# Optimization experiments

Measured on AMD Instinct MI355X. Metric: run time of the kernel, lower is better.

## Reference

```python
import jax, jax.numpy as jnp
import numpy as np

B, S, D, H = 4, 2048, 1024, 16
HD = D // H

def setup_inputs() -> dict:
    key = jax.random.key(0)
    ks = jax.random.split(key, 11)
    s = 1.0 / np.sqrt(D)
    def lin(k):
        kw, kb = jax.random.split(k)
        return (jax.random.uniform(kw, (D, D), jnp.float32, -s, s),
                jax.random.uniform(kb, (D,), jnp.float32, -s, s))
    Wq, bq = lin(ks[0]); Wk, bk = lin(ks[1]); Wv, bv = lin(ks[2]); Wo, bo = lin(ks[3])
    return {
        "query": jax.random.normal(ks[4], (B, S, D), jnp.float32),
        "key": jax.random.normal(ks[5], (B, S, D), jnp.float32),
        "value": jax.random.normal(ks[6], (B, S, D), jnp.float32),
        "Wq": Wq, "bq": bq, "Wk": Wk, "bk": bk,
        "Wv": Wv, "bv": bv, "Wo": Wo, "bo": bo,
    }

def reference(query, key, value, Wq, bq, Wk, bk, Wv, bv, Wo, bo):
    def split_heads(x):  # [B,S,D] -> [B,H,S,HD]
        return x.reshape(B, S, H, HD).transpose(0, 2, 1, 3)
    q = split_heads(query @ Wq + bq)
    k = split_heads(key @ Wk + bk)
    v = split_heads(value @ Wv + bv)
    scores = jnp.einsum('bhqd,bhkd->bhqk', q, k) / np.sqrt(HD)
    probs = jax.nn.softmax(scores, axis=-1)
    ctx = jnp.einsum('bhqk,bhkd->bhqd', probs, v)
    ctx = ctx.transpose(0, 2, 1, 3).reshape(B, S, D)
    return ctx @ Wo + bo
```

## Files before the change

### kernel.cpp

```cpp
#include <hip/hip_runtime.h>
#include <hip/hip_bf16.h>

#define B_ 4
#define S_ 2048
#define D_ 1024
#define H_ 16
#define HD_ 64
#define M_ (B_*S_)

typedef __bf16 bf16;
typedef bf16 bf16x8 __attribute__((ext_vector_type(8)));
typedef bf16 bf16x4 __attribute__((ext_vector_type(4)));
typedef bf16 bf16x2 __attribute__((ext_vector_type(2)));
typedef float f32x4 __attribute__((ext_vector_type(4)));
typedef unsigned u32x4 __attribute__((ext_vector_type(4)));

__device__ __forceinline__ void gload_lds16(const void* g, void* l) {
  __builtin_amdgcn_global_load_lds((const __attribute__((address_space(1))) void*)g,
                                   (__attribute__((address_space(3))) void*)l, 16, 0, 0);
}

__device__ __forceinline__ unsigned pk2(float a, float b) {
  bf16x2 v;
  v[0] = (bf16)a; v[1] = (bf16)b;
  return __builtin_bit_cast(unsigned, v);
}

__global__ __launch_bounds__(256)
void wtrans_kernel(const float* __restrict__ Wq, const float* __restrict__ Wk,
                   const float* __restrict__ Wv, const float* __restrict__ Wo,
                   bf16* __restrict__ Wqt, bf16* __restrict__ Wkt,
                   bf16* __restrict__ Wvt, bf16* __restrict__ Wot) {
  __shared__ float tile[64][65];
  const float* W; bf16* Wt;
  switch (blockIdx.z) {
    case 0: W = Wq; Wt = Wqt; break;
    case 1: W = Wk; Wt = Wkt; break;
    case 2: W = Wv; Wt = Wvt; break;
    default: W = Wo; Wt = Wot; break;
  }
  int n0 = blockIdx.x * 64, k0 = blockIdx.y * 64;
  int tx = threadIdx.x & 63, ty = threadIdx.x >> 6;
#pragma unroll
  for (int i = 0; i < 16; i++) {
    int k = ty + i * 4;
    tile[k][tx] = W[(size_t)(k0 + k) * D_ + n0 + tx];
  }
  __syncthreads();
#pragma unroll
  for (int i = 0; i < 16; i++) {
    int n = ty + i * 4;
    Wt[(size_t)(n0 + n) * D_ + k0 + tx] = (bf16)tile[tx][n];
  }
}

__global__ __launch_bounds__(256)
void qkv_cvt_kernel(const float* __restrict__ q, const float* __restrict__ k,
                    const float* __restrict__ v,
                    bf16* __restrict__ qo, bf16* __restrict__ ko, bf16* __restrict__ vo) {
  const float* src; bf16* dst;
  switch (blockIdx.y) {
    case 0: src = q; dst = qo; break;
    case 1: src = k; dst = ko; break;
    default: src = v; dst = vo; break;
  }
  size_t i = ((size_t)blockIdx.x * 256 + threadIdx.x) * 8;
  f32x4 a = *(const f32x4*)(src + i);
  f32x4 b = *(const f32x4*)(src + i + 4);
  bf16x8 o;
  o[0] = (bf16)a[0]; o[1] = (bf16)a[1]; o[2] = (bf16)a[2]; o[3] = (bf16)a[3];
  o[4] = (bf16)b[0]; o[5] = (bf16)b[1]; o[6] = (bf16)b[2]; o[7] = (bf16)b[3];
  *(bf16x8*)(dst + i) = o;
}

#define QSCALE 0.18033688011112042f

__global__ __launch_bounds__(256)
void proj_gemm_kernel(const bf16* __restrict__ Aqb, const bf16* __restrict__ Akb,
                      const bf16* __restrict__ Avb,
                      const bf16* __restrict__ Wqt, const bf16* __restrict__ Wkt,
                      const bf16* __restrict__ Wvt,
                      const float* __restrict__ bq, const float* __restrict__ bk,
                      const float* __restrict__ bv,
                      bf16* __restrict__ qb, bf16* __restrict__ kb, bf16* __restrict__ vbT) {
  __shared__ bf16 As[128 * 64];
  __shared__ bf16 Bs[128 * 64];
  const bf16* A; const bf16* Bt; const float* bias;
  if (blockIdx.z == 0)      { A = Aqb; Bt = Wqt; bias = bq; }
  else if (blockIdx.z == 1) { A = Akb; Bt = Wkt; bias = bk; }
  else                      { A = Avb; Bt = Wvt; bias = bv; }

  const int orig = blockIdx.y * gridDim.x + blockIdx.x;
  const int swz  = (orig & 7) * 64 + (orig >> 3);
  const int n0 = (swz & 7) * 128, m0 = (swz >> 3) * 128;

  const int tid = threadIdx.x;
  const int lane = tid & 63, w = tid >> 6;
  const int wr = w >> 1, wc = w & 1;
  const int l15 = lane & 15, quad = lane >> 4;
  const int srow = lane >> 3, schunk = lane & 7;

  f32x4 acc[4][4] = {};

  for (int kt = 0; kt < D_ / 64; kt++) {
    const int k0 = kt * 64;
#pragma unroll
    for (int t = 0; t < 4; t++) {
      int r0 = w * 32 + t * 8;
      int row = r0 + srow;
      int cg = schunk ^ (row & 7);
      gload_lds16(A + (size_t)(m0 + row) * D_ + k0 + cg * 8, &As[r0 * 64]);
      gload_lds16(Bt + (size_t)(n0 + row) * D_ + k0 + cg * 8, &Bs[r0 * 64]);
    }
    __syncthreads();

#pragma unroll
    for (int ks = 0; ks < 2; ks++) {
      bf16x8 a[4], b[4];
#pragma unroll
      for (int fm = 0; fm < 4; fm++) {
        int row = wr * 64 + fm * 16 + l15;
        a[fm] = *(const bf16x8*)(&As[row * 64 + (((ks * 4 + quad) ^ (row & 7)) * 8)]);
      }
#pragma unroll
      for (int fn = 0; fn < 4; fn++) {
        int row = wc * 64 + fn * 16 + l15;
        b[fn] = *(const bf16x8*)(&Bs[row * 64 + (((ks * 4 + quad) ^ (row & 7)) * 8)]);
      }
#pragma unroll
      for (int fm = 0; fm < 4; fm++)
#pragma unroll
        for (int fn = 0; fn < 4; fn++)
          acc[fm][fn] = __builtin_amdgcn_mfma_f32_16x16x32_bf16(a[fm], b[fn], acc[fm][fn], 0, 0, 0);
    }
    __syncthreads();
  }

  if (blockIdx.z < 2) {
    bf16* C = (blockIdx.z == 0) ? qb : kb;
    float scale = (blockIdx.z == 0) ? QSCALE : 1.0f;
#pragma unroll
    for (int fm = 0; fm < 4; fm++) {
      int row = m0 + wr * 64 + fm * 16 + quad * 4;
#pragma unroll
      for (int fn = 0; fn < 4; fn++) {
        int col = n0 + wc * 64 + fn * 16 + l15;
        float bval = bias[col];
#pragma unroll
        for (int r = 0; r < 4; r++)
          C[(size_t)(row + r) * D_ + col] = (bf16)((acc[fm][fn][r] + bval) * scale);
      }
    }
  } else {
#pragma unroll
    for (int fm = 0; fm < 4; fm++) {
      int row = m0 + wr * 64 + fm * 16 + quad * 4;
#pragma unroll
      for (int fn = 0; fn < 4; fn++) {
        int col = n0 + wc * 64 + fn * 16 + l15;
        float bval = bias[col];
        bf16x4 pk;
#pragma unroll
        for (int r = 0; r < 4; r++) pk[r] = (bf16)(acc[fm][fn][r] + bval);
        *(bf16x4*)(vbT + (size_t)col * M_ + row) = pk;
      }
    }
  }
}

#define NT_ (S_ / 64)

__global__ __launch_bounds__(256)
void attn_kernel(const bf16* __restrict__ qb, const bf16* __restrict__ kb,
                 const bf16* __restrict__ vbT, bf16* __restrict__ ctxb) {
  __shared__ bf16 Ks[2][64 * 64];
  __shared__ bf16 Vs[3][64 * 64];

  const int orig = blockIdx.y * gridDim.x + blockIdx.x;
  const int swz  = (orig & 7) * 128 + (orig >> 3);
  const int bh = swz >> 4;
  const int b = bh >> 4, h = bh & 15;
  const int q0 = (swz & 15) * 128;

  const int tid = threadIdx.x, lane = tid & 63, w = tid >> 6;
  const int l15 = lane & 15, quad = lane >> 4;

  const size_t baseQ = ((size_t)(b * S_ + q0)) * D_ + h * HD_;

  bf16x8 qf[2][2];
#pragma unroll
  for (int fm = 0; fm < 2; fm++)
#pragma unroll
    for (int ks = 0; ks < 2; ks++)
      qf[fm][ks] = *(const bf16x8*)(qb + baseQ + (size_t)(w * 32 + fm * 16 + l15) * D_ + ks * 32 + quad * 8);

  bf16x8 vones;
#pragma unroll
  for (int i = 0; i < 8; i++) vones[i] = (bf16)1.0f;

  f32x4 o[2][4] = {};
  f32x4 o_l[2] = {};

  const int srow_i = lane >> 3;
  const int schunk = lane & 7;

  auto stage = [&](int kt) {
    if (kt >= NT_) return;
    const int kbuf = kt & 1, vbuf = kt % 3;
#pragma unroll
    for (int t = 0; t < 2; t++) {
      const int r0 = w * 16 + t * 8;
      const int row = r0 + srow_i;
      const int c = schunk ^ (row & 7);
      const bf16* gK = kb + ((size_t)(b * S_ + kt * 64 + row)) * D_ + h * 64 + c * 8;
      gload_lds16(gK, &Ks[kbuf][r0 * 64]);
      const bf16* gV = vbT + ((size_t)(h * 64 + row)) * M_ + b * S_ + kt * 64 + c * 8;
      gload_lds16(gV, &Vs[vbuf][r0 * 64]);
    }
  };

  auto QK = [&](f32x4 (&st)[4][2], int kbuf) {
#pragma unroll
    for (int fk = 0; fk < 4; fk++)
#pragma unroll
      for (int fq = 0; fq < 2; fq++) st[fk][fq] = f32x4{};
    __builtin_amdgcn_s_setprio(1);
#pragma unroll
    for (int ks = 0; ks < 2; ks++) {
#pragma unroll
      for (int fk = 0; fk < 4; fk++) {
        const int key = fk * 16 + l15;
        bf16x8 kf = *(const bf16x8*)(&Ks[kbuf][key * 64 + (((ks * 4 + quad) ^ (key & 7)) * 8)]);
#pragma unroll
        for (int fq = 0; fq < 2; fq++)
          st[fk][fq] = __builtin_amdgcn_mfma_f32_16x16x32_bf16(kf, qf[fq][ks], st[fk][fq], 0, 0, 0);
      }
    }
    __builtin_amdgcn_s_setprio(0);
  };

  auto FIN = [&](f32x4 (&st)[4][2], int vbuf) {
#pragma unroll
    for (int fk = 0; fk < 4; fk++)
#pragma unroll
      for (int fq = 0; fq < 2; fq++) {
        st[fk][fq][0] = __builtin_amdgcn_exp2f(st[fk][fq][0]);
        st[fk][fq][1] = __builtin_amdgcn_exp2f(st[fk][fq][1]);
        st[fk][fq][2] = __builtin_amdgcn_exp2f(st[fk][fq][2]);
        st[fk][fq][3] = __builtin_amdgcn_exp2f(st[fk][fq][3]);
      }
#pragma unroll
    for (int ks2 = 0; ks2 < 2; ks2++) {
      bf16x8 pf[2], vf[4];
#pragma unroll
      for (int fm = 0; fm < 2; fm++) {
        unsigned A0 = pk2(st[2 * ks2][fm][0], st[2 * ks2][fm][1]);
        unsigned A1 = pk2(st[2 * ks2][fm][2], st[2 * ks2][fm][3]);
        unsigned B0 = pk2(st[2 * ks2 + 1][fm][0], st[2 * ks2 + 1][fm][1]);
        unsigned B1 = pk2(st[2 * ks2 + 1][fm][2], st[2 * ks2 + 1][fm][3]);
        auto s0 = __builtin_amdgcn_permlane32_swap(A0, B0, false, false);
        auto s1 = __builtin_amdgcn_permlane32_swap(A1, B1, false, false);
        auto t0 = __builtin_amdgcn_permlane16_swap(s0[0], s0[1], false, false);
        auto t1 = __builtin_amdgcn_permlane16_swap(s1[0], s1[1], false, false);
        u32x4 wv;
        wv[0] = t0[0]; wv[1] = t1[0]; wv[2] = t0[1]; wv[3] = t1[1];
        pf[fm] = __builtin_bit_cast(bf16x8, wv);
      }
#pragma unroll
      for (int fd = 0; fd < 4; fd++) {
        const int d = fd * 16 + l15;
        vf[fd] = *(const bf16x8*)(&Vs[vbuf][d * 64 + (((ks2 * 4 + quad) ^ (d & 7)) * 8)]);
      }
      __builtin_amdgcn_s_setprio(1);
#pragma unroll
      for (int fm = 0; fm < 2; fm++) {
#pragma unroll
        for (int fd = 0; fd < 4; fd++)
          o[fm][fd] = __builtin_amdgcn_mfma_f32_16x16x32_bf16(pf[fm], vf[fd], o[fm][fd], 0, 0, 0);
        o_l[fm] = __builtin_amdgcn_mfma_f32_16x16x32_bf16(pf[fm], vones, o_l[fm], 0, 0, 0);
      }
      __builtin_amdgcn_s_setprio(0);
    }
  };

  f32x4 stA[4][2], stB[4][2];

  stage(0);
  __syncthreads();

  for (int i = 0; i < NT_ / 2; i++) {
    const int t = 2 * i;
    stage(t + 1);
    QK(stA, t & 1);
    if (i > 0) FIN(stB, (t - 1) % 3);
    __syncthreads();
    stage(t + 2);
    QK(stB, (t + 1) & 1);
    FIN(stA, t % 3);
    __syncthreads();
  }
  FIN(stB, (NT_ - 1) % 3);

#pragma unroll
  for (int fm = 0; fm < 2; fm++) {
#pragma unroll
    for (int r = 0; r < 4; r++) {
      float inv = 1.0f / o_l[fm][r];
      int row = w * 32 + fm * 16 + quad * 4 + r;
#pragma unroll
      for (int fd = 0; fd < 4; fd++)
        ctxb[baseQ + (size_t)row * D_ + fd * 16 + l15] = (bf16)(o[fm][fd][r] * inv);
    }
  }
}

__global__ __launch_bounds__(256)
void out_gemm_kernel(const bf16* __restrict__ A, const bf16* __restrict__ Bt,
                     const float* __restrict__ bias, float* __restrict__ Cout) {
  __shared__ bf16 As[128 * 64];
  __shared__ bf16 Bs[128 * 64];
  const int orig = blockIdx.y * gridDim.x + blockIdx.x;
  const int swz  = (orig & 7) * 64 + (orig >> 3);
  const int n0 = (swz & 7) * 128, m0 = (swz >> 3) * 128;

  const int tid = threadIdx.x;
  const int lane = tid & 63, w = tid >> 6;
  const int wr = w >> 1, wc = w & 1;
  const int l15 = lane & 15, quad = lane >> 4;
  const int srow = lane >> 3, schunk = lane & 7;

  f32x4 acc[4][4] = {};

  for (int kt = 0; kt < D_ / 64; kt++) {
    const int k0 = kt * 64;
#pragma unroll
    for (int t = 0; t < 4; t++) {
      int r0 = w * 32 + t * 8;
      int row = r0 + srow;
      int cg = schunk ^ (row & 7);
      gload_lds16(A + (size_t)(m0 + row) * D_ + k0 + cg * 8, &As[r0 * 64]);
      gload_lds16(Bt + (size_t)(n0 + row) * D_ + k0 + cg * 8, &Bs[r0 * 64]);
    }
    __syncthreads();

#pragma unroll
    for (int ks = 0; ks < 2; ks++) {
      bf16x8 a[4], b[4];
#pragma unroll
      for (int fm = 0; fm < 4; fm++) {
        int row = wr * 64 + fm * 16 + l15;
        a[fm] = *(const bf16x8*)(&As[row * 64 + (((ks * 4 + quad) ^ (row & 7)) * 8)]);
      }
#pragma unroll
      for (int fn = 0; fn < 4; fn++) {
        int row = wc * 64 + fn * 16 + l15;
        b[fn] = *(const bf16x8*)(&Bs[row * 64 + (((ks * 4 + quad) ^ (row & 7)) * 8)]);
      }
#pragma unroll
      for (int fm = 0; fm < 4; fm++)
#pragma unroll
        for (int fn = 0; fn < 4; fn++)
          acc[fm][fn] = __builtin_amdgcn_mfma_f32_16x16x32_bf16(a[fm], b[fn], acc[fm][fn], 0, 0, 0);
    }
    __syncthreads();
  }
#pragma unroll
  for (int fm = 0; fm < 4; fm++) {
    int row = m0 + wr * 64 + fm * 16 + quad * 4;
#pragma unroll
    for (int fn = 0; fn < 4; fn++) {
      int col = n0 + wc * 64 + fn * 16 + l15;
      float bval = bias[col];
#pragma unroll
      for (int r = 0; r < 4; r++)
        Cout[(size_t)(row + r) * D_ + col] = acc[fm][fn][r] + bval;
    }
  }
}

extern "C" void kernel_launch(void* const* d_in, const int* in_sizes, int n_in,
                              void* d_out, int out_size, void* d_ws, size_t ws_size,
                              hipStream_t stream) {
  const float* query = (const float*)d_in[0];
  const float* key   = (const float*)d_in[1];
  const float* value = (const float*)d_in[2];
  const float* Wq = (const float*)d_in[3];
  const float* bq = (const float*)d_in[4];
  const float* Wk = (const float*)d_in[5];
  const float* bk = (const float*)d_in[6];
  const float* Wv = (const float*)d_in[7];
  const float* bv = (const float*)d_in[8];
  const float* Wo = (const float*)d_in[9];
  const float* bo = (const float*)d_in[10];
  float* out = (float*)d_out;

  char* ws = (char*)d_ws;
  const size_t WT_BYTES = (size_t)D_ * D_ * sizeof(bf16);
  const size_t MD_BYTES = (size_t)M_ * D_ * sizeof(bf16);
  bf16* Wqt  = (bf16*)(ws);
  bf16* Wkt  = (bf16*)(ws + WT_BYTES);
  bf16* Wvt  = (bf16*)(ws + 2 * WT_BYTES);
  bf16* Wot  = (bf16*)(ws + 3 * WT_BYTES);
  bf16* qb   = (bf16*)(ws + 4 * WT_BYTES);
  bf16* kb   = (bf16*)(ws + 4 * WT_BYTES + MD_BYTES);
  bf16* vbT  = (bf16*)(ws + 4 * WT_BYTES + 2 * MD_BYTES);
  bf16* ctxb = (bf16*)(ws + 4 * WT_BYTES + 3 * MD_BYTES);
  bf16* qcv  = ctxb;
  bf16* kcv  = (bf16*)(ws + 4 * WT_BYTES + 4 * MD_BYTES);
  bf16* vcv  = (bf16*)(ws + 4 * WT_BYTES + 5 * MD_BYTES);

  wtrans_kernel<<<dim3(D_ / 64, D_ / 64, 4), 256, 0, stream>>>(
      Wq, Wk, Wv, Wo, Wqt, Wkt, Wvt, Wot);

  qkv_cvt_kernel<<<dim3((size_t)M_ * D_ / 2048, 3), 256, 0, stream>>>(
      query, key, value, qcv, kcv, vcv);

  proj_gemm_kernel<<<dim3(D_ / 128, M_ / 128, 3), 256, 0, stream>>>(
      qcv, kcv, vcv, Wqt, Wkt, Wvt, bq, bk, bv, qb, kb, vbT);

  attn_kernel<<<dim3(S_ / 128, B_ * H_), 256, 0, stream>>>(qb, kb, vbT, ctxb);

  out_gemm_kernel<<<dim3(D_ / 128, M_ / 128), 256, 0, stream>>>(ctxb, Wot, bo, out);
}
```

Measured before the change: 334.4 us.

## Fuse fp32-to-bf16 input conversion into projection GEMM A-tile loading

Removes the separate qkv conversion kernel. The projection GEMM now reads fp32 activations directly into registers, converts them to bf16 and writes them into swizzled LDS, with a register prefetch of the next k-tile that overlaps the MFMA compute. This avoids writing and re-reading three bf16 copies of the inputs and saves one kernel launch. In exchange, each GEMM tile reads twice the bytes of A from global memory because every N-tile reloads fp32, the kernel needs more registers, and there are two barriers per iteration.

```diff
diff --git a/kernel.cpp b/kernel.cpp
--- a/kernel.cpp
+++ b/kernel.cpp
@@ -54,30 +54,11 @@
   }
 }
 
+#define QSCALE 0.18033688011112042f
+
 __global__ __launch_bounds__(256)
-void qkv_cvt_kernel(const float* __restrict__ q, const float* __restrict__ k,
-                    const float* __restrict__ v,
-                    bf16* __restrict__ qo, bf16* __restrict__ ko, bf16* __restrict__ vo) {
-  const float* src; bf16* dst;
-  switch (blockIdx.y) {
-    case 0: src = q; dst = qo; break;
-    case 1: src = k; dst = ko; break;
-    default: src = v; dst = vo; break;
-  }
-  size_t i = ((size_t)blockIdx.x * 256 + threadIdx.x) * 8;
-  f32x4 a = *(const f32x4*)(src + i);
-  f32x4 b = *(const f32x4*)(src + i + 4);
-  bf16x8 o;
-  o[0] = (bf16)a[0]; o[1] = (bf16)a[1]; o[2] = (bf16)a[2]; o[3] = (bf16)a[3];
-  o[4] = (bf16)b[0]; o[5] = (bf16)b[1]; o[6] = (bf16)b[2]; o[7] = (bf16)b[3];
-  *(bf16x8*)(dst + i) = o;
-}
-
-#define QSCALE 0.18033688011112042f
-
-__global__ __launch_bounds__(256)
-void proj_gemm_kernel(const bf16* __restrict__ Aqb, const bf16* __restrict__ Akb,
-                      const bf16* __restrict__ Avb,
+void proj_gemm_kernel(const float* __restrict__ Aq, const float* __restrict__ Ak,
+                      const float* __restrict__ Av,
                       const bf16* __restrict__ Wqt, const bf16* __restrict__ Wkt,
                       const bf16* __restrict__ Wvt,
                       const float* __restrict__ bq, const float* __restrict__ bk,
@@ -85,10 +66,10 @@
                       bf16* __restrict__ qb, bf16* __restrict__ kb, bf16* __restrict__ vbT) {
   __shared__ bf16 As[128 * 64];
   __shared__ bf16 Bs[128 * 64];
-  const bf16* A; const bf16* Bt; const float* bias;
-  if (blockIdx.z == 0)      { A = Aqb; Bt = Wqt; bias = bq; }
-  else if (blockIdx.z == 1) { A = Akb; Bt = Wkt; bias = bk; }
-  else                      { A = Avb; Bt = Wvt; bias = bv; }
+  const float* A; const bf16* Bt; const float* bias;
+  if (blockIdx.z == 0)      { A = Aq; Bt = Wqt; bias = bq; }
+  else if (blockIdx.z == 1) { A = Ak; Bt = Wkt; bias = bk; }
+  else                      { A = Av; Bt = Wvt; bias = bv; }
 
   const int orig = blockIdx.y * gridDim.x + blockIdx.x;
   const int swz  = (orig & 7) * 64 + (orig >> 3);
@@ -99,21 +80,40 @@
   const int wr = w >> 1, wc = w & 1;
   const int l15 = lane & 15, quad = lane >> 4;
   const int srow = lane >> 3, schunk = lane & 7;
+  const int arow4 = lane >> 4, c4 = lane & 15;
 
   f32x4 acc[4][4] = {};
-
-  for (int kt = 0; kt < D_ / 64; kt++) {
+  f32x4 ar[8];
+
+  auto loadA = [&](int kt) {
+    const int k0 = kt * 64;
+#pragma unroll
+    for (int t = 0; t < 8; t++) {
+      int row = w * 32 + t * 4 + arow4;
+      ar[t] = *(const f32x4*)(A + (size_t)(m0 + row) * D_ + k0 + c4 * 4);
+    }
+  };
+  auto writeA = [&]() {
+#pragma unroll
+    for (int t = 0; t < 8; t++) {
+      int row = w * 32 + t * 4 + arow4;
+      bf16x4 pk;
+      pk[0] = (bf16)ar[t][0]; pk[1] = (bf16)ar[t][1];
+      pk[2] = (bf16)ar[t][2]; pk[3] = (bf16)ar[t][3];
+      *(bf16x4*)(&As[row * 64 + (((c4 >> 1) ^ (row & 7)) * 8 + (c4 & 1) * 4)]) = pk;
+    }
+  };
+  auto stageB = [&](int kt) {
     const int k0 = kt * 64;
 #pragma unroll
     for (int t = 0; t < 4; t++) {
       int r0 = w * 32 + t * 8;
       int row = r0 + srow;
       int cg = schunk ^ (row & 7);
-      gload_lds16(A + (size_t)(m0 + row) * D_ + k0 + cg * 8, &As[r0 * 64]);
       gload_lds16(Bt + (size_t)(n0 + row) * D_ + k0 + cg * 8, &Bs[r0 * 64]);
     }
-    __syncthreads();
-
+  };
+  auto compute = [&]() {
 #pragma unroll
     for (int ks = 0; ks < 2; ks++) {
       bf16x8 a[4], b[4];
@@ -132,6 +132,19 @@
 #pragma unroll
         for (int fn = 0; fn < 4; fn++)
           acc[fm][fn] = __builtin_amdgcn_mfma_f32_16x16x32_bf16(a[fm], b[fn], acc[fm][fn], 0, 0, 0);
+    }
+  };
+
+  constexpr int KT = D_ / 64;
+  loadA(0); stageB(0); writeA();
+  __syncthreads();
+  for (int kt = 0; kt < KT; kt++) {
+    if (kt + 1 < KT) loadA(kt + 1);
+    compute();
+    __syncthreads();
+    if (kt + 1 < KT) {
+      stageB(kt + 1);
+      writeA();
     }
     __syncthreads();
   }
@@ -405,18 +418,12 @@
   bf16* kb   = (bf16*)(ws + 4 * WT_BYTES + MD_BYTES);
   bf16* vbT  = (bf16*)(ws + 4 * WT_BYTES + 2 * MD_BYTES);
   bf16* ctxb = (bf16*)(ws + 4 * WT_BYTES + 3 * MD_BYTES);
-  bf16* qcv  = ctxb;
-  bf16* kcv  = (bf16*)(ws + 4 * WT_BYTES + 4 * MD_BYTES);
-  bf16* vcv  = (bf16*)(ws + 4 * WT_BYTES + 5 * MD_BYTES);
 
   wtrans_kernel<<<dim3(D_ / 64, D_ / 64, 4), 256, 0, stream>>>(
       Wq, Wk, Wv, Wo, Wqt, Wkt, Wvt, Wot);
 
-  qkv_cvt_kernel<<<dim3((size_t)M_ * D_ / 2048, 3), 256, 0, stream>>>(
-      query, key, value, qcv, kcv, vcv);
-
   proj_gemm_kernel<<<dim3(D_ / 128, M_ / 128, 3), 256, 0, stream>>>(
-      qcv, kcv, vcv, Wqt, Wkt, Wvt, bq, bk, bv, qb, kb, vbT);
+      query, key, value, Wqt, Wkt, Wvt, bq, bk, bv, qb, kb, vbT);
 
   attn_kernel<<<dim3(S_ / 128, B_ * H_), 256, 0, stream>>>(qb, kb, vbT, ctxb);
 
```

Measured after the change: 348.8 us. 4.3% more time.
